# Kernel optimization log

Hardware: AMD Instinct MI355X
Metric: run time of the kernel (lower is better)

Reference implementation:

```python
import jax, jax.numpy as jnp
import numpy as np

B, N_IN, N_HID, T = 64, 512, 512, 512


def setup_inputs() -> dict:
    key = jax.random.key(0)
    k1, k2, k3, k4, k5 = jax.random.split(key, 5)
    scale = 1.0 / np.sqrt(N_HID).astype(np.float32)
    return {
        "X": jax.random.normal(k1, (B, N_IN, T), dtype=jnp.float32),
        "Wax": jax.random.normal(k2, (N_IN, N_HID), dtype=jnp.float32) * scale,
        "Waa": jax.random.normal(k3, (N_HID, N_HID), dtype=jnp.float32) * scale,
        "bx": jax.random.normal(k4, (N_HID,), dtype=jnp.float32) * scale,
        "ba": jax.random.normal(k5, (N_HID,), dtype=jnp.float32) * scale,
    }


def reference(X, Wax, Waa, bx, ba):
    # X: [B, n_in, T]. a_{t+1} = tanh(x_t @ Wax + bx + a_t @ Waa + ba)
    # Precompute the input projections for all timesteps in one big GEMM:
    # [T, B, n_hid]
    Xt = jnp.transpose(X, (2, 0, 1))  # [T, B, n_in]
    inp_proj = jnp.einsum('tbi,ih->tbh', Xt, Wax) + bx + ba

    def step(a, u):
        a_next = jnp.tanh(u + a @ Waa)
        return a_next, a_next

    a0 = jnp.zeros((X.shape[0], Waa.shape[0]), dtype=X.dtype)
    _, A = jax.lax.scan(step, a0, inp_proj)
    return A  # [T, B, n_hid] == stacked A[1:] of the torch module
```

## Files before the change

kernel.cpp:

```cpp
#include <hip/hip_runtime.h>
#include <math.h>

#define BB   64
#define NIN  512
#define NH   512
#define TT   512

typedef _Float16 half2_t __attribute__((ext_vector_type(2)));
typedef _Float16 half8_t __attribute__((ext_vector_type(8)));
typedef float    f32x4  __attribute__((ext_vector_type(4)));

__device__ __forceinline__ unsigned pk16(float x, float y) {
    unsigned lo = (unsigned)__builtin_bit_cast(unsigned short, (_Float16)x);
    unsigned hi = (unsigned)__builtin_bit_cast(unsigned short, (_Float16)y);
    return lo | (hi << 16);
}

__device__ __forceinline__ float dot2u(unsigned w, unsigned a, float acc) {
    return __builtin_amdgcn_fdot2(__builtin_bit_cast(half2_t, w),
                                  __builtin_bit_cast(half2_t, a), acc, false);
}

__device__ __forceinline__ float tanh_fast(float x) {
    float ax = __builtin_fabsf(x);
    float e  = __builtin_amdgcn_exp2f(-2.885390082f * ax);
    float r  = (1.0f - e) * __builtin_amdgcn_rcpf(1.0f + e);
    return __builtin_copysignf(r, x);
}

__global__ __launch_bounds__(256) void inp_proj_mfma(
    const float* __restrict__ X, const float* __restrict__ Wax,
    const float* __restrict__ bx, const float* __restrict__ ba,
    float* __restrict__ out)
{
    __shared__ unsigned Xsp[16][132];
    __shared__ unsigned Wsp[16][132];

    const int b   = blockIdx.z;
    const int t0  = blockIdx.y * 128;
    const int h0  = blockIdx.x * 128;
    const int tid = threadIdx.x;
    const int lane = tid & 63;
    const int wid  = tid >> 6;
    const int wm   = wid >> 1;
    const int wn   = wid & 1;
    const int q    = lane >> 4;
    const int r16  = lane & 15;

    const int lr = tid >> 4;
    const int lc = (tid & 15) * 8;

    const float* Xb = X + (size_t)b * NIN * TT;

    f32x4 acc[4][4] = {};

    for (int i0 = 0; i0 < NIN; i0 += 32) {
        const int k0 = i0 + 2 * lr, k1 = k0 + 1;
        float4 xa0 = *(const float4*)&Xb[(size_t)k0 * TT + t0 + lc];
        float4 xa1 = *(const float4*)&Xb[(size_t)k0 * TT + t0 + lc + 4];
        float4 xb0 = *(const float4*)&Xb[(size_t)k1 * TT + t0 + lc];
        float4 xb1 = *(const float4*)&Xb[(size_t)k1 * TT + t0 + lc + 4];
        float4 wa0 = *(const float4*)&Wax[(size_t)k0 * NH + h0 + lc];
        float4 wa1 = *(const float4*)&Wax[(size_t)k0 * NH + h0 + lc + 4];
        float4 wb0 = *(const float4*)&Wax[(size_t)k1 * NH + h0 + lc];
        float4 wb1 = *(const float4*)&Wax[(size_t)k1 * NH + h0 + lc + 4];

        uint4 xp0, xp1, wp0, wp1;
        xp0.x = pk16(xa0.x, xb0.x); xp0.y = pk16(xa0.y, xb0.y);
        xp0.z = pk16(xa0.z, xb0.z); xp0.w = pk16(xa0.w, xb0.w);
        xp1.x = pk16(xa1.x, xb1.x); xp1.y = pk16(xa1.y, xb1.y);
        xp1.z = pk16(xa1.z, xb1.z); xp1.w = pk16(xa1.w, xb1.w);
        wp0.x = pk16(wa0.x, wb0.x); wp0.y = pk16(wa0.y, wb0.y);
        wp0.z = pk16(wa0.z, wb0.z); wp0.w = pk16(wa0.w, wb0.w);
        wp1.x = pk16(wa1.x, wb1.x); wp1.y = pk16(wa1.y, wb1.y);
        wp1.z = pk16(wa1.z, wb1.z); wp1.w = pk16(wa1.w, wb1.w);

        __syncthreads();
        *(uint4*)&Xsp[lr][lc]     = xp0;
        *(uint4*)&Xsp[lr][lc + 4] = xp1;
        *(uint4*)&Wsp[lr][lc]     = wp0;
        *(uint4*)&Wsp[lr][lc + 4] = wp1;
        __syncthreads();

        uint4 af[4], bf[4];
#pragma unroll
        for (int mt = 0; mt < 4; ++mt) {
            const int tc = wm * 64 + mt * 16 + r16;
            af[mt].x = Xsp[4 * q + 0][tc];
            af[mt].y = Xsp[4 * q + 1][tc];
            af[mt].z = Xsp[4 * q + 2][tc];
            af[mt].w = Xsp[4 * q + 3][tc];
        }
#pragma unroll
        for (int nt = 0; nt < 4; ++nt) {
            const int hc = wn * 64 + nt * 16 + r16;
            bf[nt].x = Wsp[4 * q + 0][hc];
            bf[nt].y = Wsp[4 * q + 1][hc];
            bf[nt].z = Wsp[4 * q + 2][hc];
            bf[nt].w = Wsp[4 * q + 3][hc];
        }
#pragma unroll
        for (int mt = 0; mt < 4; ++mt)
#pragma unroll
            for (int nt = 0; nt < 4; ++nt)
                acc[mt][nt] = __builtin_amdgcn_mfma_f32_16x16x32_f16(
                    __builtin_bit_cast(half8_t, af[mt]),
                    __builtin_bit_cast(half8_t, bf[nt]),
                    acc[mt][nt], 0, 0, 0);
    }

#pragma unroll
    for (int nt = 0; nt < 4; ++nt) {
        const int h = h0 + wn * 64 + nt * 16 + r16;
        const float bias = bx[h] + ba[h];
#pragma unroll
        for (int mt = 0; mt < 4; ++mt) {
            const int trow = t0 + wm * 64 + mt * 16 + q * 4;
#pragma unroll
            for (int rr = 0; rr < 4; ++rr) {
                out[(size_t)(trow + rr) * (BB * NH) + (size_t)b * NH + h] =
                    acc[mt][nt][rr] + bias;
            }
        }
    }
}

#define NRP 52
#define NLP 12
#define PSTRIDE 516

__device__ __forceinline__ unsigned bline(unsigned a, int l) {
    return (unsigned)__builtin_amdgcn_readlane((int)a, l);
}

__global__ __launch_bounds__(512, 2) void rnn_scan_v5(
    const float* __restrict__ Waa, float* __restrict__ out)
{
    __shared__ unsigned wlds[NLP * 4][NH];
    __shared__ unsigned a_lds[2][256];
    __shared__ float    part[4][PSTRIDE];

    const int tid  = threadIdx.x;
    const int b    = blockIdx.x;
    const int cidx = tid & 127;
    const int kq   = tid >> 7;
    const int h4   = cidx * 4;
    const int lane = tid & 63;

    unsigned w0[NRP], w1[NRP], w2[NRP], w3[NRP];
#pragma unroll
    for (int j = 0; j < NRP; ++j) {
        const int k = kq * 128 + 2 * j;
        float4 r0 = *(const float4*)&Waa[(size_t)k       * NH + h4];
        float4 r1 = *(const float4*)&Waa[(size_t)(k + 1) * NH + h4];
        w0[j] = pk16(r0.x, r1.x);
        w1[j] = pk16(r0.y, r1.y);
        w2[j] = pk16(r0.z, r1.z);
        w3[j] = pk16(r0.w, r1.w);
    }
#pragma unroll
    for (int p = 0; p < NLP; ++p) {
        const int k = kq * 128 + 2 * (NRP + p);
        float4 r0 = *(const float4*)&Waa[(size_t)k       * NH + h4];
        float4 r1 = *(const float4*)&Waa[(size_t)(k + 1) * NH + h4];
        wlds[p * 4 + 0][tid] = pk16(r0.x, r1.x);
        wlds[p * 4 + 1][tid] = pk16(r0.y, r1.y);
        wlds[p * 4 + 2][tid] = pk16(r0.z, r1.z);
        wlds[p * 4 + 3][tid] = pk16(r0.w, r1.w);
    }

    if (tid < 256) a_lds[0][tid] = 0u;
    __syncthreads();

    float* ob = out + (size_t)b * NH + tid;
    float u_cur = ob[0];

    for (int t = 0; t < TT; ++t) {
        const int tn = (t + 1 < TT) ? (t + 1) : (TT - 1);
        float u_next = ob[(size_t)tn * (BB * NH)];

        unsigned a_loc = a_lds[t & 1][kq * 64 + lane];

        float acc0 = 0.f, acc1 = 0.f, acc2 = 0.f, acc3 = 0.f;
#pragma unroll
        for (int j = 0; j < NRP; j += 2) {
            unsigned ra = bline(a_loc, j);
            unsigned rb = bline(a_loc, j + 1);
            acc0 = dot2u(w0[j], ra, acc0);
            acc1 = dot2u(w1[j], ra, acc1);
            acc2 = dot2u(w2[j], ra, acc2);
            acc3 = dot2u(w3[j], ra, acc3);
            acc0 = dot2u(w0[j + 1], rb, acc0);
            acc1 = dot2u(w1[j + 1], rb, acc1);
            acc2 = dot2u(w2[j + 1], rb, acc2);
            acc3 = dot2u(w3[j + 1], rb, acc3);
        }
#pragma unroll
        for (int p = 0; p < NLP; ++p) {
            unsigned ra = bline(a_loc, NRP + p);
            unsigned v0 = wlds[p * 4 + 0][tid];
            unsigned v1 = wlds[p * 4 + 1][tid];
            unsigned v2 = wlds[p * 4 + 2][tid];
            unsigned v3 = wlds[p * 4 + 3][tid];
            acc0 = dot2u(v0, ra, acc0);
            acc1 = dot2u(v1, ra, acc1);
            acc2 = dot2u(v2, ra, acc2);
            acc3 = dot2u(v3, ra, acc3);
        }

        float4 pv; pv.x = acc0; pv.y = acc1; pv.z = acc2; pv.w = acc3;
        *(float4*)&part[kq][h4] = pv;
        __builtin_amdgcn_s_waitcnt(0xC07F);
        __builtin_amdgcn_s_barrier();

        float x = u_cur + ((part[0][tid] + part[1][tid]) +
                           (part[2][tid] + part[3][tid]));
        float an = tanh_fast(x);
        ob[(size_t)t * (BB * NH)] = an;
        u_cur = u_next;

        ((unsigned short*)a_lds[(t + 1) & 1])[tid] =
            __builtin_bit_cast(unsigned short, (_Float16)an);
        __builtin_amdgcn_s_waitcnt(0xC07F);
        __builtin_amdgcn_s_barrier();
    }
}

extern "C" void kernel_launch(void* const* d_in, const int* in_sizes, int n_in,
                              void* d_out, int out_size, void* d_ws, size_t ws_size,
                              hipStream_t stream) {
    const float* X   = (const float*)d_in[0];
    const float* Wax = (const float*)d_in[1];
    const float* Waa = (const float*)d_in[2];
    const float* bx  = (const float*)d_in[3];
    const float* ba  = (const float*)d_in[4];
    float* out = (float*)d_out;

    dim3 g1(NH / 128, TT / 128, BB);
    inp_proj_mfma<<<g1, 256, 0, stream>>>(X, Wax, bx, ba, out);
    rnn_scan_v5<<<BB, NH, 0, stream>>>(Waa, out);
}
```

Baseline: 1.012 ms.

## Split recurrent scan K-reduction across 1024 threads with 8-way partial sums

The recurrent scan kernel now launches 1024 threads per batch block instead of 512. Each 128-thread group handles 64 rows of Waa rather than 128, which halves the serial dot2 chain per thread per timestep. The 8 partial sums are reduced through LDS by the first 512 threads. The LDS-resident weights are also stored as uint4 so each step does one vector load instead of four scalar ones. The cost is a wider reduction, idle threads during the tanh phase, and register pressure under the new launch bounds, which could force spills.

```diff
diff --git a/kernel.cpp b/kernel.cpp
--- a/kernel.cpp
+++ b/kernel.cpp
@@ -125,32 +125,32 @@
     }
 }
 
-#define NRP 52
-#define NLP 12
+#define NRP 24
+#define NLP 8
 #define PSTRIDE 516
 
 __device__ __forceinline__ unsigned bline(unsigned a, int l) {
     return (unsigned)__builtin_amdgcn_readlane((int)a, l);
 }
 
-__global__ __launch_bounds__(512, 2) void rnn_scan_v5(
+__global__ __launch_bounds__(1024, 4) void rnn_scan_v6(
     const float* __restrict__ Waa, float* __restrict__ out)
 {
-    __shared__ unsigned wlds[NLP * 4][NH];
+    __shared__ uint4    wldsv[NLP][1024];
     __shared__ unsigned a_lds[2][256];
-    __shared__ float    part[4][PSTRIDE];
+    __shared__ float    part[8][PSTRIDE];
 
     const int tid  = threadIdx.x;
     const int b    = blockIdx.x;
     const int cidx = tid & 127;
     const int kq   = tid >> 7;
     const int h4   = cidx * 4;
-    const int lane = tid & 63;
+    const int l32  = tid & 31;
 
     unsigned w0[NRP], w1[NRP], w2[NRP], w3[NRP];
 #pragma unroll
     for (int j = 0; j < NRP; ++j) {
-        const int k = kq * 128 + 2 * j;
+        const int k = kq * 64 + 2 * j;
         float4 r0 = *(const float4*)&Waa[(size_t)k       * NH + h4];
         float4 r1 = *(const float4*)&Waa[(size_t)(k + 1) * NH + h4];
         w0[j] = pk16(r0.x, r1.x);
@@ -160,26 +160,30 @@
     }
 #pragma unroll
     for (int p = 0; p < NLP; ++p) {
-        const int k = kq * 128 + 2 * (NRP + p);
+        const int k = kq * 64 + 2 * (NRP + p);
         float4 r0 = *(const float4*)&Waa[(size_t)k       * NH + h4];
         float4 r1 = *(const float4*)&Waa[(size_t)(k + 1) * NH + h4];
-        wlds[p * 4 + 0][tid] = pk16(r0.x, r1.x);
-        wlds[p * 4 + 1][tid] = pk16(r0.y, r1.y);
-        wlds[p * 4 + 2][tid] = pk16(r0.z, r1.z);
-        wlds[p * 4 + 3][tid] = pk16(r0.w, r1.w);
+        uint4 wv;
+        wv.x = pk16(r0.x, r1.x);
+        wv.y = pk16(r0.y, r1.y);
+        wv.z = pk16(r0.z, r1.z);
+        wv.w = pk16(r0.w, r1.w);
+        wldsv[p][tid] = wv;
     }
 
     if (tid < 256) a_lds[0][tid] = 0u;
     __syncthreads();
 
-    float* ob = out + (size_t)b * NH + tid;
-    float u_cur = ob[0];
+    const int  hc  = tid & 511;
+    const bool red = (tid < 512);
+    float* ob = out + (size_t)b * NH + hc;
+    float u_cur = red ? ob[0] : 0.0f;
 
     for (int t = 0; t < TT; ++t) {
         const int tn = (t + 1 < TT) ? (t + 1) : (TT - 1);
-        float u_next = ob[(size_t)tn * (BB * NH)];
-
-        unsigned a_loc = a_lds[t & 1][kq * 64 + lane];
+        float u_next = red ? ob[(size_t)tn * (BB * NH)] : 0.0f;
+
+        unsigned a_loc = a_lds[t & 1][kq * 32 + l32];
 
         float acc0 = 0.f, acc1 = 0.f, acc2 = 0.f, acc3 = 0.f;
 #pragma unroll
@@ -198,14 +202,11 @@
 #pragma unroll
         for (int p = 0; p < NLP; ++p) {
             unsigned ra = bline(a_loc, NRP + p);
-            unsigned v0 = wlds[p * 4 + 0][tid];
-            unsigned v1 = wlds[p * 4 + 1][tid];
-            unsigned v2 = wlds[p * 4 + 2][tid];
-            unsigned v3 = wlds[p * 4 + 3][tid];
-            acc0 = dot2u(v0, ra, acc0);
-            acc1 = dot2u(v1, ra, acc1);
-            acc2 = dot2u(v2, ra, acc2);
-            acc3 = dot2u(v3, ra, acc3);
+            uint4 v = wldsv[p][tid];
+            acc0 = dot2u(v.x, ra, acc0);
+            acc1 = dot2u(v.y, ra, acc1);
+            acc2 = dot2u(v.z, ra, acc2);
+            acc3 = dot2u(v.w, ra, acc3);
         }
 
         float4 pv; pv.x = acc0; pv.y = acc1; pv.z = acc2; pv.w = acc3;
@@ -213,14 +214,16 @@
         __builtin_amdgcn_s_waitcnt(0xC07F);
         __builtin_amdgcn_s_barrier();
 
-        float x = u_cur + ((part[0][tid] + part[1][tid]) +
-                           (part[2][tid] + part[3][tid]));
-        float an = tanh_fast(x);
-        ob[(size_t)t * (BB * NH)] = an;
+        if (red) {
+            float x = u_cur +
+                (((part[0][hc] + part[1][hc]) + (part[2][hc] + part[3][hc])) +
+                 ((part[4][hc] + part[5][hc]) + (part[6][hc] + part[7][hc])));
+            float an = tanh_fast(x);
+            ob[(size_t)t * (BB * NH)] = an;
+            ((unsigned short*)a_lds[(t + 1) & 1])[hc] =
+                __builtin_bit_cast(unsigned short, (_Float16)an);
+        }
         u_cur = u_next;
-
-        ((unsigned short*)a_lds[(t + 1) & 1])[tid] =
-            __builtin_bit_cast(unsigned short, (_Float16)an);
         __builtin_amdgcn_s_waitcnt(0xC07F);
         __builtin_amdgcn_s_barrier();
     }
@@ -238,5 +241,5 @@
 
     dim3 g1(NH / 128, TT / 128, BB);
     inp_proj_mfma<<<g1, 256, 0, stream>>>(X, Wax, bx, ba, out);
-    rnn_scan_v5<<<BB, NH, 0, stream>>>(Waa, out);
-}
+    rnn_scan_v6<<<BB, 1024, 0, stream>>>(Waa, out);
+}
```

Result: faster. 972.8 us (-3.8%).
